# Kernel tuning notes

Hardware: AMD Instinct MI355X
Metric: run time of the kernel (lower is better)

The kernel has to match this reference:

```python
import jax, jax.numpy as jnp
import numpy as np


def _ortho_matrix(key, d, m):
    # block-orthogonal random matrix with chi-distributed row-norm rescaling
    n_blocks = m // d + (1 if m % d else 0)
    keys = jax.random.split(key, n_blocks + 1)
    blocks = []
    for i in range(m // d):
        q, _ = jnp.linalg.qr(jax.random.normal(keys[i], (d, d), dtype=jnp.float32))
        blocks.append(q)
    rem = m % d
    if rem > 0:
        q, _ = jnp.linalg.qr(jax.random.normal(keys[m // d], (d, d), dtype=jnp.float32))
        blocks.append(q[:, :rem])
    proj = jnp.concatenate(blocks, axis=1)  # [d, m]
    scales = jnp.linalg.norm(jax.random.normal(keys[-1], (m, d), dtype=jnp.float32), axis=1)
    return proj * scales[None, :]


def _feature_map(x, P, eps=1e-6):
    # FAVOR+ positive softmax feature map: [exp(xP - |x|^2/2), exp(-xP - |x|^2/2)]
    proj = x @ P  # [B,N,m]
    xn = 0.5 * jnp.sum(x * x, axis=-1, keepdims=True)
    pos = proj - xn
    neg = -proj - xn
    mx = jnp.maximum(jnp.max(pos, axis=-1, keepdims=True), jnp.max(neg, axis=-1, keepdims=True))
    feats = jnp.concatenate([jnp.exp(pos - mx), jnp.exp(neg - mx)], axis=-1)
    return feats * (2.0 * P.shape[1]) ** -0.5 + eps  # [B,N,2m]


def setup_inputs() -> dict:
    key = jax.random.key(0)
    ks = jax.random.split(key, 16)
    B, C, N = 4, 256, 8192
    da, nb = C // 4, 64
    d_geo, r_geo = 16, 16
    x = jax.random.normal(ks[0], (B, C, N), dtype=jnp.float32)
    pos = jax.random.uniform(ks[1], (B, N, 3), dtype=jnp.float32)
    Wq = jax.random.normal(ks[2], (da, C), dtype=jnp.float32) * (C ** -0.5)
    Wk = jax.random.normal(ks[3], (da, C), dtype=jnp.float32) * (C ** -0.5)
    Wv = jax.random.normal(ks[4], (C, C), dtype=jnp.float32) * (C ** -0.5)
    proj_sm = _ortho_matrix(ks[5], da, nb)  # [da, nb]
    Wg1 = jax.random.normal(ks[6], (d_geo, 3), dtype=jnp.float32) * (3 ** -0.5)
    bg1 = jnp.zeros((d_geo,), dtype=jnp.float32)
    Wg2 = jax.random.normal(ks[7], (d_geo, d_geo), dtype=jnp.float32) * (d_geo ** -0.5)
    bg2 = jnp.zeros((d_geo,), dtype=jnp.float32)
    log_tau = jnp.zeros((), dtype=jnp.float32)
    omega_geo = _ortho_matrix(ks[8], d_geo, r_geo)  # [d_geo, r_geo]
    Wp = jax.random.normal(ks[9], (C, C), dtype=jnp.float32) * (C ** -0.5)
    bn_gamma = jnp.ones((C,), dtype=jnp.float32)
    bn_beta = jnp.zeros((C,), dtype=jnp.float32)
    return {"x": x, "pos": pos, "Wq": Wq, "Wk": Wk, "Wv": Wv, "proj_sm": proj_sm,
            "Wg1": Wg1, "bg1": bg1, "Wg2": Wg2, "bg2": bg2, "log_tau": log_tau,
            "omega_geo": omega_geo, "Wp": Wp, "bn_gamma": bn_gamma, "bn_beta": bn_beta}


def reference(x, pos, Wq, Wk, Wv, proj_sm, Wg1, bg1, Wg2, bg2, log_tau, omega_geo, Wp, bn_gamma, bn_beta):
    eps = 1e-6
    da = Wq.shape[0]
    scale = da ** -0.25
    # 1x1 convs == channel matmuls; transpose to [B,N,*]
    q = jnp.einsum('bcn,oc->bno', x, Wq) * scale
    k = jnp.einsum('bcn,oc->bno', x, Wk) * scale
    v = jnp.einsum('bcn,oc->bno', x, Wv)
    q_p = _feature_map(q, proj_sm, eps)  # [B,N,r_sm]
    k_p = _feature_map(k, proj_sm, eps)
    # GeoRFF: learnable Gaussian RFF on MLP-transformed coordinates
    g = jax.nn.relu(pos @ Wg1.T + bg1) @ Wg2.T + bg2  # [B,N,d_geo]
    tau = jax.nn.softplus(log_tau) + 1e-6
    z = jnp.sqrt(2.0 * tau) * g
    z_proj = z @ omega_geo  # [B,N,r_geo]
    z_norm = 0.5 * jnp.sum(z * z, axis=-1, keepdims=True)
    phi = jnp.exp(z_proj - z_norm) * (omega_geo.shape[1] ** -0.5)  # [B,N,r_geo]
    # outer-product feature combination
    B, N, r_sm = q_p.shape
    r_geo = phi.shape[-1]
    Phi_q = (q_p[..., :, None] * phi[..., None, :]).reshape(B, N, r_sm * r_geo)
    Phi_k = (k_p[..., :, None] * phi[..., None, :]).reshape(B, N, r_sm * r_geo)
    # O(N) linear-attention chain
    kv = jnp.einsum('bnr,bnc->brc', Phi_k, v)         # [B,r,C]
    k_sum = jnp.sum(Phi_k, axis=1)                     # [B,r]
    denom = jnp.einsum('bnr,br->bn', Phi_q, k_sum)[..., None] + eps
    fsa = jnp.einsum('bnr,brc->bnc', Phi_q, kv) / denom  # [B,N,C]
    # offset attention: proj(x - fsa) + x, proj = Conv1x1 -> BN(train stats) -> ReLU
    y = x - jnp.transpose(fsa, (0, 2, 1))  # [B,C,N]
    h = jnp.einsum('bcn,oc->bon', y, Wp)
    mean = jnp.mean(h, axis=(0, 2), keepdims=True)
    var = jnp.var(h, axis=(0, 2), keepdims=True)
    hn = (h - mean) * jax.lax.rsqrt(var + 1e-5) * bn_gamma[None, :, None] + bn_beta[None, :, None]
    return jax.nn.relu(hn) + x
```

## Files before the change

kernel.cpp:

```cpp
#include <hip/hip_runtime.h>
#include <hip/hip_bf16.h>
#include <math.h>

#define BB 4
#define CC 256
#define NN 8192
#define RSM 128
#define RGEO 16

typedef __attribute__((ext_vector_type(8))) short short8v;
typedef __attribute__((ext_vector_type(4))) float f32x4;
typedef __attribute__((ext_vector_type(4))) unsigned int u32x4;

#define MFMA16 __builtin_amdgcn_mfma_f32_16x16x32_bf16

#define P_QP   0ull
#define P_KPT  8388608ull
#define P_PHIR 16777216ull
#define P_PHIT 17825792ull
#define P_XT   18874368ull
#define P_VT   35651584ull
#define P_YNT  35651584ull
#define P_KVT  52428800ull
#define P_KVF  56623104ull
#define P_KSUM 65011712ull
#define P_DEN  65044480ull
#define P_WQK  65175552ull
#define P_WV   65241088ull
#define P_WP   65372160ull
#define P_PSMT 65503232ull
#define P_BN   65511424ull
#define P_H    0ull

__device__ __forceinline__ unsigned short f2bu(float f){
    __hip_bfloat16 h = __float2bfloat16(f);
    return __builtin_bit_cast(unsigned short, h);
}
__device__ __forceinline__ float bu2f(unsigned short u){
    return __builtin_bit_cast(float, ((unsigned int)u) << 16);
}
__device__ __forceinline__ unsigned int pack2(float a, float b){
    return (unsigned int)f2bu(a) | (((unsigned int)f2bu(b)) << 16);
}
__device__ __forceinline__ int swz128(int row, int cb){ return (row*128 + cb) ^ ((row & 7) << 4); }
__device__ __forceinline__ int swz256(int row, int cb){ return (row*256 + cb) ^ ((row & 7) << 4); }

__device__ __forceinline__ unsigned int bmul2(unsigned int uk, unsigned int up, float& ksacc){
    float lo = __builtin_bit_cast(float, uk << 16) * __builtin_bit_cast(float, up << 16);
    float hi = __builtin_bit_cast(float, uk & 0xffff0000u) * __builtin_bit_cast(float, up & 0xffff0000u);
    ksacc += lo + hi;
    return pack2(lo, hi);
}

__device__ __forceinline__ void stage64(const unsigned short* __restrict__ g, size_t stride,
                                        char* lds, int t){
    #pragma unroll
    for (int i = 0; i < 2; ++i){
        int id = t + 256*i; int row = id >> 3, q = id & 7;
        short8v v = *(const short8v*)(g + (size_t)row*stride + q*8);
        *(short8v*)(lds + swz128(row, q*16)) = v;
    }
}
__device__ __forceinline__ short8v fld(const char* lds, int row, int cb){
    return *(const short8v*)(lds + swz128(row, cb));
}
__device__ __forceinline__ void mfma8(const char* As, const char* Bs, f32x4 acc[2][2],
                                      int wm, int wn, int lr, int lq){
    #pragma unroll
    for (int kk = 0; kk < 2; ++kk){
        short8v a0 = fld(As, wm*32 + lr,      kk*64 + lq*16);
        short8v a1 = fld(As, wm*32 + 16 + lr, kk*64 + lq*16);
        short8v b0 = fld(Bs, wn*32 + lr,      kk*64 + lq*16);
        short8v b1 = fld(Bs, wn*32 + 16 + lr, kk*64 + lq*16);
        acc[0][0] = MFMA16(a0, b0, acc[0][0], 0, 0, 0);
        acc[0][1] = MFMA16(a0, b1, acc[0][1], 0, 0, 0);
        acc[1][0] = MFMA16(a1, b0, acc[1][0], 0, 0, 0);
        acc[1][1] = MFMA16(a1, b1, acc[1][1], 0, 0, 0);
    }
}
__device__ __forceinline__ void mfma16s(const char* As, const char* Bs, f32x4 acc[4][4],
                                        int wm, int wn, int lr, int lq){
    #pragma unroll
    for (int kk = 0; kk < 2; ++kk){
        short8v af[4], bf[4];
        #pragma unroll
        for (int f = 0; f < 4; ++f) af[f] = fld(As, wm*64 + f*16 + lr, kk*64 + lq*16);
        #pragma unroll
        for (int f = 0; f < 4; ++f) bf[f] = fld(Bs, wn*64 + f*16 + lr, kk*64 + lq*16);
        #pragma unroll
        for (int fa = 0; fa < 4; ++fa)
            #pragma unroll
            for (int fb = 0; fb < 4; ++fb)
                acc[fa][fb] = MFMA16(af[fa], bf[fb], acc[fa][fb], 0, 0, 0);
    }
}
__device__ __forceinline__ void mfma4x2(const char* As, const char* Bs, f32x4 acc[4][2],
                                        int wm, int wn, int lr, int lq){
    #pragma unroll
    for (int kk = 0; kk < 2; ++kk){
        short8v af[4], bf[2];
        #pragma unroll
        for (int f = 0; f < 4; ++f) af[f] = fld(As, wm*64 + f*16 + lr, kk*64 + lq*16);
        #pragma unroll
        for (int f = 0; f < 2; ++f) bf[f] = fld(Bs, wn*32 + f*16 + lr, kk*64 + lq*16);
        #pragma unroll
        for (int fa = 0; fa < 4; ++fa)
            #pragma unroll
            for (int fb = 0; fb < 2; ++fb)
                acc[fa][fb] = MFMA16(af[fa], bf[fb], acc[fa][fb], 0, 0, 0);
    }
}

__global__ __launch_bounds__(256) void k_prep(const float* __restrict__ Wq, const float* __restrict__ Wk,
    const float* __restrict__ Wv, const float* __restrict__ Wp, const float* __restrict__ Psm,
    unsigned short* __restrict__ Wqk_bf, unsigned short* __restrict__ Wv_bf,
    unsigned short* __restrict__ Wp_bf, unsigned short* __restrict__ Psm_t)
{
    const int tid = blockIdx.x*256 + threadIdx.x;
    const int nth = 64*256;
    for (int i = tid; i < 32768; i += nth){
        int o = i >> 8, c = i & 255;
        Wqk_bf[i] = f2bu(o < 64 ? Wq[o*256 + c] : Wk[(o-64)*256 + c]);
    }
    for (int i = tid; i < 65536; i += nth) Wv_bf[i] = f2bu(Wv[i]);
    for (int i = tid; i < 65536; i += nth) Wp_bf[i] = f2bu(Wp[i]);
    for (int i = tid; i < 4096; i += nth){
        int m = i >> 6, o = i & 63;
        Psm_t[i] = f2bu(Psm[o*64 + m] * 0.35355339059327373f);
    }
}

__global__ __launch_bounds__(256) void k_xt(const float* __restrict__ x, unsigned short* __restrict__ xT)
{
    __shared__ float xs[64][65];
    const int t = threadIdx.x;
    const int b  = blockIdx.x >> 9;
    const int ct = (blockIdx.x >> 7) & 3;
    const int nt = blockIdx.x & 127;
    const int c0 = ct*64, n0 = nt*64;
    #pragma unroll
    for (int i = 0; i < 4; ++i){
        int id = t + 256*i; int row = id >> 4, fq = id & 15;
        f32x4 v = *(const f32x4*)(x + ((size_t)(b*CC + c0 + row))*NN + n0 + fq*4);
        xs[row][fq*4+0] = v[0]; xs[row][fq*4+1] = v[1];
        xs[row][fq*4+2] = v[2]; xs[row][fq*4+3] = v[3];
    }
    __syncthreads();
    #pragma unroll
    for (int i = 0; i < 2; ++i){
        int id = t + 256*i; int n = id >> 3, q = id & 7;
        u32x4 o;
        #pragma unroll
        for (int j2 = 0; j2 < 4; ++j2)
            o[j2] = pack2(xs[q*8 + j2*2][n], xs[q*8 + j2*2+1][n]);
        *(u32x4*)(void*)(xT + ((size_t)(b*NN + n0 + n))*CC + c0 + q*8) = o;
    }
}

__global__ __launch_bounds__(256) void k_wgemm(const unsigned short* __restrict__ A,
    const unsigned short* __restrict__ Bsrc, unsigned short* __restrict__ out, int orows)
{
    __shared__ __align__(16) char As[8192];
    __shared__ __align__(16) char Bs[8192];
    const int t = threadIdx.x;
    const int l = t & 63, w = t >> 6, wm = w >> 1, wn = w & 1, lr = l & 15, lq = l >> 4;
    const int b  = blockIdx.x >> 9;
    const int ct = (blockIdx.x >> 7) & 3;
    const int nt = blockIdx.x & 127;
    const int c0 = ct*64, n0 = nt*64;

    f32x4 acc[2][2] = {};
    for (int ks = 0; ks < 4; ++ks){
        stage64(A + (size_t)c0*256 + ks*64, 256, As, t);
        stage64(Bsrc + ((size_t)(b*NN + n0))*256 + ks*64, 256, Bs, t);
        __syncthreads();
        mfma8(As, Bs, acc, wm, wn, lr, lq);
        __syncthreads();
    }
    #pragma unroll
    for (int mi = 0; mi < 2; ++mi)
        #pragma unroll
        for (int ni = 0; ni < 2; ++ni)
            #pragma unroll
            for (int r = 0; r < 4; ++r){
                int c = c0 + wm*32 + mi*16 + lq*4 + r;
                int n = n0 + wn*32 + ni*16 + lr;
                out[((size_t)(b*orows + c))*NN + n] = f2bu(acc[mi][ni][r]);
            }
}

__global__ __launch_bounds__(256) void k_qk(const unsigned short* __restrict__ Wqk,
    const unsigned short* __restrict__ xT, const unsigned short* __restrict__ Psm_t,
    unsigned short* __restrict__ qp, unsigned short* __restrict__ kp_t)
{
    __shared__ __align__(16) char As[16384];
    __shared__ __align__(16) char Bs[8192];
    __shared__ __align__(16) char Ts[16384];
    __shared__ __align__(16) char Ps[8192];
    const int t = threadIdx.x;
    const int l = t & 63, w = t >> 6, wm = w >> 1, wn = w & 1, lr = l & 15, lq = l >> 4;
    const int b  = blockIdx.x >> 7;
    const int nt = blockIdx.x & 127;
    const int n0 = nt*64;

    stage64(Psm_t, 64, Ps, t);

    f32x4 acc[4][2] = {};
    for (int ks = 0; ks < 4; ++ks){
        #pragma unroll
        for (int i = 0; i < 4; ++i){
            int id = t + 256*i; int row = id >> 3, q = id & 7;
            short8v v = *(const short8v*)(Wqk + (size_t)row*256 + ks*64 + q*8);
            *(short8v*)(As + swz128(row, q*16)) = v;
        }
        stage64(xT + ((size_t)(b*NN + n0))*256 + ks*64, 256, Bs, t);
        __syncthreads();
        #pragma unroll
        for (int kk = 0; kk < 2; ++kk){
            short8v b0 = fld(Bs, wn*32 + lr,      kk*64 + lq*16);
            short8v b1 = fld(Bs, wn*32 + 16 + lr, kk*64 + lq*16);
            #pragma unroll
            for (int mi = 0; mi < 4; ++mi){
                short8v a = fld(As, wm*64 + mi*16 + lr, kk*64 + lq*16);
                acc[mi][0] = MFMA16(a, b0, acc[mi][0], 0, 0, 0);
                acc[mi][1] = MFMA16(a, b1, acc[mi][1], 0, 0, 0);
            }
        }
        __syncthreads();
    }
    #pragma unroll
    for (int mi = 0; mi < 4; ++mi)
        #pragma unroll
        for (int ni = 0; ni < 2; ++ni){
            int op = (wm*64 + mi*16 + lq*4)*2;
            int nrow = wn*32 + ni*16 + lr;
            *(unsigned int*)(Ts + swz256(nrow, op))     = pack2(acc[mi][ni][0], acc[mi][ni][1]);
            *(unsigned int*)(Ts + swz256(nrow, op + 4)) = pack2(acc[mi][ni][2], acc[mi][ni][3]);
        }
    __syncthreads();

    const float inv128 = 0.08838834764831845f;
    for (int p = 0; p < 2; ++p){
        f32x4 ac[4] = {};
        #pragma unroll
        for (int kk = 0; kk < 2; ++kk){
            short8v bf = *(const short8v*)(Ts + swz256(w*16 + lr, p*128 + kk*64 + lq*16));
            #pragma unroll
            for (int mi = 0; mi < 4; ++mi){
                short8v a = *(const short8v*)(Ps + swz128(mi*16 + lr, kk*64 + lq*16));
                ac[mi] = MFMA16(a, bf, ac[mi], 0, 0, 0);
            }
        }
        float mx = 0.f;
        #pragma unroll
        for (int mi = 0; mi < 4; ++mi)
            #pragma unroll
            for (int r = 0; r < 4; ++r) mx = fmaxf(mx, fabsf(ac[mi][r]));
        mx = fmaxf(mx, __shfl_xor(mx, 16));
        mx = fmaxf(mx, __shfl_xor(mx, 32));
        const int n = n0 + w*16 + lr;
        if (p == 0){
            unsigned short* qr = qp + ((size_t)(b*NN + n))*RSM;
            #pragma unroll
            for (int mi = 0; mi < 4; ++mi){
                float e0 = __expf( ac[mi][0]-mx)*inv128 + 1e-6f;
                float e1 = __expf( ac[mi][1]-mx)*inv128 + 1e-6f;
                float e2 = __expf( ac[mi][2]-mx)*inv128 + 1e-6f;
                float e3 = __expf( ac[mi][3]-mx)*inv128 + 1e-6f;
                float g0 = __expf(-ac[mi][0]-mx)*inv128 + 1e-6f;
                float g1 = __expf(-ac[mi][1]-mx)*inv128 + 1e-6f;
                float g2 = __expf(-ac[mi][2]-mx)*inv128 + 1e-6f;
                float g3 = __expf(-ac[mi][3]-mx)*inv128 + 1e-6f;
                int i0 = mi*16 + lq*4;
                uint2 pu; pu.x = pack2(e0, e1); pu.y = pack2(e2, e3);
                uint2 nu; nu.x = pack2(g0, g1); nu.y = pack2(g2, g3);
                *(uint2*)(void*)(qr + i0)      = pu;
                *(uint2*)(void*)(qr + 64 + i0) = nu;
            }
        } else {
            unsigned short* kb = kp_t + (size_t)(b*RSM)*NN + n;
            #pragma unroll
            for (int mi = 0; mi < 4; ++mi){
                int i0 = mi*16 + lq*4;
                #pragma unroll
                for (int r = 0; r < 4; ++r){
                    kb[(size_t)(i0 + r)*NN]      = f2bu(__expf( ac[mi][r]-mx)*inv128 + 1e-6f);
                    kb[(size_t)(i0 + r + 64)*NN] = f2bu(__expf(-ac[mi][r]-mx)*inv128 + 1e-6f);
                }
            }
        }
    }
}

__global__ __launch_bounds__(256) void k_phi(const float* __restrict__ pos,
    const float* __restrict__ Wg1, const float* __restrict__ bg1,
    const float* __restrict__ Wg2, const float* __restrict__ bg2,
    const float* __restrict__ log_tau, const float* __restrict__ omega,
    unsigned short* __restrict__ phi_row, unsigned short* __restrict__ phi_t)
{
    const int t = threadIdx.x;
    const int b = blockIdx.x >> 5;
    const int n = ((blockIdx.x & 31) << 8) + t;
    const float* pp = pos + ((size_t)(b*NN + n))*3;
    const float p0 = pp[0], p1 = pp[1], p2 = pp[2];
    float hb[16];
    #pragma unroll
    for (int i = 0; i < 16; ++i)
        hb[i] = fmaxf(0.f, fmaf(Wg1[i*3+0], p0, fmaf(Wg1[i*3+1], p1, fmaf(Wg1[i*3+2], p2, bg1[i]))));
    const float tau = log1pf(__expf(log_tau[0])) + 1e-6f;
    const float sc  = sqrtf(2.f*tau);
    float z[16]; float zn = 0.f;
    #pragma unroll
    for (int i = 0; i < 16; ++i){
        float g = bg2[i];
        #pragma unroll
        for (int j = 0; j < 16; ++j) g = fmaf(Wg2[i*16+j], hb[j], g);
        z[i] = sc*g; zn = fmaf(z[i], z[i], zn);
    }
    zn *= 0.5f;
    float val[16];
    #pragma unroll
    for (int m = 0; m < 16; ++m){
        float s = 0.f;
        #pragma unroll
        for (int i = 0; i < 16; ++i) s = fmaf(z[i], omega[i*16+m], s);
        val[m] = __expf(s - zn)*0.25f;
    }
    unsigned short* pr = phi_row + ((size_t)(b*NN + n))*16;
    u32x4 o0, o1;
    #pragma unroll
    for (int j2 = 0; j2 < 4; ++j2){
        o0[j2] = pack2(val[j2*2], val[j2*2+1]);
        o1[j2] = pack2(val[8+j2*2], val[8+j2*2+1]);
    }
    *(u32x4*)(void*)pr = o0;
    *(u32x4*)(void*)(pr + 8) = o1;
    #pragma unroll
    for (int m = 0; m < 16; ++m)
        phi_t[((size_t)(b*RGEO + m))*NN + n] = f2bu(val[m]);
}

__global__ __launch_bounds__(256) void k_kv(const unsigned short* __restrict__ kp_t,
    const unsigned short* __restrict__ phi_t, const unsigned short* __restrict__ v_t,
    float* __restrict__ kv_f32, float* __restrict__ ksum)
{
    __shared__ __align__(16) char As[16384];
    __shared__ __align__(16) char Bs[16384];
    const int t = threadIdx.x;
    const int l = t & 63, w = t >> 6, wm = w >> 1, wn = w & 1, lr = l & 15, lq = l >> 4;
    const int bid = blockIdx.x;
    const int rt  = bid & 15;
    const int ct  = (bid >> 4) & 1;
    const int ksl = (bid >> 5) & 15;
    const int b   = bid >> 9;
    const int c0 = ct*128, r0 = rt*128;

    const int arow = t >> 3, aq = t & 7;
    const int brow = t >> 1, half = t & 1;
    const int rg = r0 + brow;
    const unsigned short* kpr = kp_t + ((size_t)(b*RSM  + (rg >> 4)))*NN;
    const unsigned short* phr = phi_t + ((size_t)(b*RGEO + (rg & 15)))*NN;
    const unsigned short* vb  = v_t + ((size_t)(b*CC + c0))*NN;
    float ksacc = 0.f;

    short8v vA[4];
    unsigned int ob[16];
    int nk = ksl*512;

    #pragma unroll
    for (int i = 0; i < 4; ++i)
        vA[i] = *(const short8v*)(vb + (size_t)(arow + 32*i)*NN + nk + aq*8);
    #pragma unroll
    for (int g2 = 0; g2 < 4; ++g2){
        u32x4 uk = __builtin_bit_cast(u32x4, *(const short8v*)(kpr + nk + half*32 + g2*8));
        u32x4 up = __builtin_bit_cast(u32x4, *(const short8v*)(phr + nk + half*32 + g2*8));
        #pragma unroll
        for (int j = 0; j < 4; ++j) ob[g2*4 + j] = bmul2(uk[j], up[j], ksacc);
    }

    f32x4 acc[4][4] = {};
    for (int ks = 0; ks < 8; ++ks){
        __syncthreads();
        #pragma unroll
        for (int i = 0; i < 4; ++i)
            *(short8v*)(As + swz128(arow + 32*i, aq*16)) = vA[i];
        #pragma unroll
        for (int g2 = 0; g2 < 4; ++g2){
            u32x4 o; o[0]=ob[g2*4]; o[1]=ob[g2*4+1]; o[2]=ob[g2*4+2]; o[3]=ob[g2*4+3];
            *(u32x4*)(Bs + swz128(brow, half*64 + g2*16)) = o;
        }
        if (ks < 7){
            nk += 64;
            #pragma unroll
            for (int i = 0; i < 4; ++i)
                vA[i] = *(const short8v*)(vb + (size_t)(arow + 32*i)*NN + nk + aq*8);
            #pragma unroll
            for (int g2 = 0; g2 < 4; ++g2){
                u32x4 uk = __builtin_bit_cast(u32x4, *(const short8v*)(kpr + nk + half*32 + g2*8));
                u32x4 up = __builtin_bit_cast(u32x4, *(const short8v*)(phr + nk + half*32 + g2*8));
                #pragma unroll
                for (int j = 0; j < 4; ++j) ob[g2*4 + j] = bmul2(uk[j], up[j], ksacc);
            }
        }
        __syncthreads();
        mfma16s(As, Bs, acc, wm, wn, lr, lq);
    }
    #pragma unroll
    for (int fa = 0; fa < 4; ++fa)
        #pragma unroll
        for (int fb = 0; fb < 4; ++fb)
            #pragma unroll
            for (int e = 0; e < 4; ++e){
                int c = c0 + wm*64 + fa*16 + lq*4 + e;
                int r = r0 + wn*64 + fb*16 + lr;
                atomicAdd(&kv_f32[((size_t)(b*CC + c))*2048 + r], acc[fa][fb][e]);
            }
    if (ct == 0){
        float o = __shfl_xor(ksacc, 1);
        if (half == 0) atomicAdd(&ksum[b*2048 + rg], ksacc + o);
    }
}

__global__ __launch_bounds__(256) void k_kvred(const float* __restrict__ kv_f32,
    unsigned short* __restrict__ kv_t)
{
    const size_t i = ((size_t)blockIdx.x*256 + threadIdx.x)*4;
    f32x4 v = *(const f32x4*)(kv_f32 + i);
    uint2 o; o.x = pack2(v[0], v[1]); o.y = pack2(v[2], v[3]);
    *(uint2*)(void*)(kv_t + i) = o;
}

__global__ __launch_bounds__(256) void k_denom(const unsigned short* __restrict__ qp,
    const unsigned short* __restrict__ phi_row, const float* __restrict__ ksum,
    float* __restrict__ den)
{
    __shared__ float ks[2048];
    const int t = threadIdx.x;
    const int b = blockIdx.x >> 5;
    const int n = ((blockIdx.x & 31) << 8) + t;
    const float* ksrc = ksum + b*2048;
    #pragma unroll
    for (int i = 0; i < 8; ++i){ int idx = t + 256*i; ks[idx] = ksrc[idx]; }
    __syncthreads();
    float phf[16];
    {
        const unsigned short* pr = phi_row + ((size_t)(b*NN + n))*16;
        short8v a = *(const short8v*)pr;
        short8v c = *(const short8v*)(pr + 8);
        #pragma unroll
        for (int j = 0; j < 8; ++j){ phf[j] = bu2f((unsigned short)a[j]); phf[8+j] = bu2f((unsigned short)c[j]); }
    }
    const unsigned short* qr = qp + ((size_t)(b*NN + n))*RSM;
    float acc = 0.f;
    for (int i = 0; i < 128; i += 8){
        short8v qv = *(const short8v*)(qr + i);
        #pragma unroll
        for (int ii = 0; ii < 8; ++ii){
            const float* kk = &ks[(i + ii)*16];
            float s = 0.f;
            #pragma unroll
            for (int j = 0; j < 16; ++j) s = fmaf(phf[j], kk[j], s);
            acc = fmaf(bu2f((unsigned short)qv[ii]), s, acc);
        }
    }
    den[b*NN + n] = acc + 1e-6f;
}

__global__ __launch_bounds__(256) void k_fsa(const unsigned short* __restrict__ kv_t,
    const unsigned short* __restrict__ qp, const unsigned short* __restrict__ phi_row,
    const float* __restrict__ den, const unsigned short* __restrict__ xT,
    unsigned short* __restrict__ y_nt)
{
    __shared__ __align__(16) char Sm[24576];
    char* As = Sm;
    char* Bs = Sm + 16384;
    const int t = threadIdx.x;
    const int l = t & 63, w = t >> 6, wm = w >> 1, wn = w & 1, lr = l & 15, lq = l >> 4;
    const int nt = blockIdx.x & 127;
    const int ct = (blockIdx.x >> 7) & 1;
    const int b  = blockIdx.x >> 8;
    const int c0 = ct*128, n0 = nt*64;

    const int arow = t >> 3, aq = t & 7;
    const int brow = t >> 2, quarter = t & 3;
    float phf[16];
    {
        const unsigned short* pr = phi_row + ((size_t)(b*NN + n0 + brow))*16;
        short8v a = *(const short8v*)pr;
        short8v c = *(const short8v*)(pr + 8);
        #pragma unroll
        for (int j = 0; j < 8; ++j){ phf[j] = bu2f((unsigned short)a[j]); phf[8+j] = bu2f((unsigned short)c[j]); }
    }
    const unsigned short* qrow = qp + ((size_t)(b*NN + n0 + brow))*RSM;
    const unsigned short* kvb  = kv_t + ((size_t)(b*CC + c0))*2048;

    short8v vA[4];
    float qv;
    int rk = 0;
    #pragma unroll
    for (int i = 0; i < 4; ++i)
        vA[i] = *(const short8v*)(kvb + (size_t)(arow + 32*i)*2048 + rk + aq*8);
    qv = bu2f(qrow[(rk >> 4) + quarter]);

    f32x4 acc[4][2] = {};
    for (int ks = 0; ks < 32; ++ks){
        u32x4 o0, o1;
        #pragma unroll
        for (int j2 = 0; j2 < 4; ++j2){
            o0[j2] = pack2(qv*phf[j2*2],     qv*phf[j2*2+1]);
            o1[j2] = pack2(qv*phf[8+j2*2],   qv*phf[8+j2*2+1]);
        }
        __syncthreads();
        #pragma unroll
        for (int i = 0; i < 4; ++i)
            *(short8v*)(As + swz128(arow + 32*i, aq*16)) = vA[i];
        *(u32x4*)(Bs + swz128(brow, quarter*32))      = o0;
        *(u32x4*)(Bs + swz128(brow, quarter*32 + 16)) = o1;
        if (ks < 31){
            rk += 64;
            #pragma unroll
            for (int i = 0; i < 4; ++i)
                vA[i] = *(const short8v*)(kvb + (size_t)(arow + 32*i)*2048 + rk + aq*8);
            qv = bu2f(qrow[(rk >> 4) + quarter]);
        }
        __syncthreads();
        mfma4x2(As, Bs, acc, wm, wn, lr, lq);
    }
    __syncthreads();
    float rd[2];
    #pragma unroll
    for (int fb = 0; fb < 2; ++fb)
        rd[fb] = 1.0f / den[(size_t)b*NN + n0 + wn*32 + fb*16 + lr];
    #pragma unroll
    for (int fa = 0; fa < 4; ++fa)
        #pragma unroll
        for (int fb = 0; fb < 2; ++fb){
            int nrow = wn*32 + fb*16 + lr;
            int cb   = (wm*64 + fa*16 + lq*4)*2;
            *(unsigned int*)(Sm + swz256(nrow, cb))     = pack2(acc[fa][fb][0]*rd[fb], acc[fa][fb][1]*rd[fb]);
            *(unsigned int*)(Sm + swz256(nrow, cb + 4)) = pack2(acc[fa][fb][2]*rd[fb], acc[fa][fb][3]*rd[fb]);
        }
    __syncthreads();
    #pragma unroll
    for (int i = 0; i < 4; ++i){
        int id = t + 256*i; int row = id >> 4, q = id & 15;
        short8v fs = *(const short8v*)(Sm + swz256(row, q*16));
        short8v xv = *(const short8v*)(xT + ((size_t)(b*NN + n0 + row))*CC + c0 + q*8);
        u32x4 o;
        #pragma unroll
        for (int j2 = 0; j2 < 4; ++j2){
            float y0 = bu2f((unsigned short)xv[j2*2])   - bu2f((unsigned short)fs[j2*2]);
            float y1 = bu2f((unsigned short)xv[j2*2+1]) - bu2f((unsigned short)fs[j2*2+1]);
            o[j2] = pack2(y0, y1);
        }
        *(u32x4*)(void*)(y_nt + ((size_t)(b*NN + n0 + row))*CC + c0 + q*8) = o;
    }
}

__global__ __launch_bounds__(256) void k_bnstat(const unsigned short* __restrict__ h,
    const float* __restrict__ gamma, const float* __restrict__ beta, float* __restrict__ bn)
{
    __shared__ float s1[256], s2[256];
    const int t = threadIdx.x, c = blockIdx.x;
    float a1 = 0.f, a2 = 0.f;
    for (int b = 0; b < 4; ++b){
        const unsigned short* hr = h + ((size_t)(b*CC + c))*NN;
        #pragma unroll
        for (int i = 0; i < 4; ++i){
            short8v v = *(const short8v*)(hr + (t + i*256)*8);
            #pragma unroll
            for (int j = 0; j < 8; ++j){ float f = bu2f((unsigned short)v[j]); a1 += f; a2 = fmaf(f, f, a2); }
        }
    }
    s1[t] = a1; s2[t] = a2; __syncthreads();
    for (int st = 128; st > 0; st >>= 1){
        if (t < st){ s1[t] += s1[t + st]; s2[t] += s2[t + st]; }
        __syncthreads();
    }
    if (t == 0){
        float inv = 1.f/32768.f;
        float mean = s1[0]*inv, var = s2[0]*inv - mean*mean;
        float sc = gamma[c]*rsqrtf(var + 1e-5f);
        bn[512 + c] = sc; bn[768 + c] = fmaf(-mean, sc, beta[c]);
    }
}

__global__ __launch_bounds__(256) void k_apply(const unsigned short* __restrict__ h,
    const float* __restrict__ x, const float* __restrict__ bn, float* __restrict__ out)
{
    const size_t tot8 = (size_t)BB*CC*NN/8;
    for (size_t i = (size_t)blockIdx.x*256 + threadIdx.x; i < tot8; i += 2048*256){
        int c = (int)((i >> 10) & 255);
        float s = bn[512 + c], bb = bn[768 + c];
        short8v hv = *(const short8v*)(h + i*8);
        f32x4 x0 = *(const f32x4*)(x + i*8);
        f32x4 x1 = *(const f32x4*)(x + i*8 + 4);
        f32x4 o0, o1;
        #pragma unroll
        for (int j = 0; j < 4; ++j){
            o0[j] = fmaxf(fmaf(bu2f((unsigned short)hv[j]),     s, bb), 0.f) + x0[j];
            o1[j] = fmaxf(fmaf(bu2f((unsigned short)hv[4 + j]), s, bb), 0.f) + x1[j];
        }
        *(f32x4*)(out + i*8)     = o0;
        *(f32x4*)(out + i*8 + 4) = o1;
    }
}

extern "C" void kernel_launch(void* const* d_in, const int* in_sizes, int n_in,
                              void* d_out, int out_size, void* d_ws, size_t ws_size,
                              hipStream_t stream)
{
    (void)in_sizes; (void)n_in; (void)out_size; (void)ws_size;
    const float* x       = (const float*)d_in[0];
    const float* pos     = (const float*)d_in[1];
    const float* Wq      = (const float*)d_in[2];
    const float* Wk      = (const float*)d_in[3];
    const float* Wv      = (const float*)d_in[4];
    const float* Psm     = (const float*)d_in[5];
    const float* Wg1     = (const float*)d_in[6];
    const float* bg1     = (const float*)d_in[7];
    const float* Wg2     = (const float*)d_in[8];
    const float* bg2     = (const float*)d_in[9];
    const float* log_tau = (const float*)d_in[10];
    const float* omega   = (const float*)d_in[11];
    const float* Wp      = (const float*)d_in[12];
    const float* gamma   = (const float*)d_in[13];
    const float* beta    = (const float*)d_in[14];
    char* W = (char*)d_ws;
    float* out = (float*)d_out;

    unsigned short* qp    = (unsigned short*)(W + P_QP);
    unsigned short* kp_t  = (unsigned short*)(W + P_KPT);
    unsigned short* phir  = (unsigned short*)(W + P_PHIR);
    unsigned short* phit  = (unsigned short*)(W + P_PHIT);
    unsigned short* xT    = (unsigned short*)(W + P_XT);
    unsigned short* v_t   = (unsigned short*)(W + P_VT);
    unsigned short* y_nt  = (unsigned short*)(W + P_YNT);
    unsigned short* kv_t  = (unsigned short*)(W + P_KVT);
    float*          kvf   = (float*)(W + P_KVF);
    float*          ksum  = (float*)(W + P_KSUM);
    float*          den   = (float*)(W + P_DEN);
    unsigned short* Wqk_b = (unsigned short*)(W + P_WQK);
    unsigned short* Wv_b  = (unsigned short*)(W + P_WV);
    unsigned short* Wp_b  = (unsigned short*)(W + P_WP);
    unsigned short* Psm_t = (unsigned short*)(W + P_PSMT);
    float*          bn    = (float*)(W + P_BN);
    unsigned short* hbuf  = (unsigned short*)(W + P_H);

    hipMemsetAsync(W + P_KVF, 0, 8421376, stream);
    k_prep  <<<  64, 256, 0, stream>>>(Wq, Wk, Wv, Wp, Psm, Wqk_b, Wv_b, Wp_b, Psm_t);
    k_xt    <<<2048, 256, 0, stream>>>(x, xT);
    k_wgemm <<<2048, 256, 0, stream>>>(Wv_b, xT, v_t, 256);
    k_qk    <<< 512, 256, 0, stream>>>(Wqk_b, xT, Psm_t, qp, kp_t);
    k_phi   <<< 128, 256, 0, stream>>>(pos, Wg1, bg1, Wg2, bg2, log_tau, omega, phir, phit);
    k_kv    <<<2048, 256, 0, stream>>>(kp_t, phit, v_t, kvf, ksum);
    k_kvred <<<2048, 256, 0, stream>>>(kvf, kv_t);
    k_denom <<< 128, 256, 0, stream>>>(qp, phir, ksum, den);
    k_fsa   <<<1024, 256, 0, stream>>>(kv_t, qp, phir, den, xT, y_nt);
    k_wgemm <<<2048, 256, 0, stream>>>(Wp_b, y_nt, hbuf, 256);
    k_bnstat<<< 256, 256, 0, stream>>>(hbuf, gamma, beta, bn);
    k_apply <<<2048, 256, 0, stream>>>(hbuf, x, bn, out);
}
```

Before: 353.3 us.

## Fuse denominator into fsa kernel and halve kv split-K blocks

Removes the separate k_denom kernel. Each k_fsa block now loads ksum into shared memory, accumulates the denominator from the same q·phi products it already builds for the MFMA operand, and reduces it across lanes with shuffles. Separately, k_kv now covers 1024 tokens per block instead of 512 and launches half as many blocks, which halves the atomicAdd traffic into the fp32 kv buffer. The cost is extra per-iteration FMAs and 8KB more LDS in fsa, which may lower occupancy, plus a longer serial loop with fewer blocks in k_kv.

```diff
diff --git a/kernel.cpp b/kernel.cpp
--- a/kernel.cpp
+++ b/kernel.cpp
@@ -24,7 +24,6 @@
 #define P_KVT  52428800ull
 #define P_KVF  56623104ull
 #define P_KSUM 65011712ull
-#define P_DEN  65044480ull
 #define P_WQK  65175552ull
 #define P_WV   65241088ull
 #define P_WP   65372160ull
@@ -351,8 +350,8 @@
     const int bid = blockIdx.x;
     const int rt  = bid & 15;
     const int ct  = (bid >> 4) & 1;
-    const int ksl = (bid >> 5) & 15;
-    const int b   = bid >> 9;
+    const int ksl = (bid >> 5) & 7;
+    const int b   = bid >> 8;
     const int c0 = ct*128, r0 = rt*128;
 
     const int arow = t >> 3, aq = t & 7;
@@ -365,7 +364,7 @@
 
     short8v vA[4];
     unsigned int ob[16];
-    int nk = ksl*512;
+    int nk = ksl*1024;
 
     #pragma unroll
     for (int i = 0; i < 4; ++i)
@@ -379,7 +378,7 @@
     }
 
     f32x4 acc[4][4] = {};
-    for (int ks = 0; ks < 8; ++ks){
+    for (int ks = 0; ks < 16; ++ks){
         __syncthreads();
         #pragma unroll
         for (int i = 0; i < 4; ++i)
@@ -389,7 +388,7 @@
             u32x4 o; o[0]=ob[g2*4]; o[1]=ob[g2*4+1]; o[2]=ob[g2*4+2]; o[3]=ob[g2*4+3];
             *(u32x4*)(Bs + swz128(brow, half*64 + g2*16)) = o;
         }
-        if (ks < 7){
+        if (ks < 15){
             nk += 64;
             #pragma unroll
             for (int i = 0; i < 4; ++i)
@@ -430,48 +429,14 @@
     *(uint2*)(void*)(kv_t + i) = o;
 }
 
-__global__ __launch_bounds__(256) void k_denom(const unsigned short* __restrict__ qp,
-    const unsigned short* __restrict__ phi_row, const float* __restrict__ ksum,
-    float* __restrict__ den)
-{
-    __shared__ float ks[2048];
-    const int t = threadIdx.x;
-    const int b = blockIdx.x >> 5;
-    const int n = ((blockIdx.x & 31) << 8) + t;
-    const float* ksrc = ksum + b*2048;
-    #pragma unroll
-    for (int i = 0; i < 8; ++i){ int idx = t + 256*i; ks[idx] = ksrc[idx]; }
-    __syncthreads();
-    float phf[16];
-    {
-        const unsigned short* pr = phi_row + ((size_t)(b*NN + n))*16;
-        short8v a = *(const short8v*)pr;
-        short8v c = *(const short8v*)(pr + 8);
-        #pragma unroll
-        for (int j = 0; j < 8; ++j){ phf[j] = bu2f((unsigned short)a[j]); phf[8+j] = bu2f((unsigned short)c[j]); }
-    }
-    const unsigned short* qr = qp + ((size_t)(b*NN + n))*RSM;
-    float acc = 0.f;
-    for (int i = 0; i < 128; i += 8){
-        short8v qv = *(const short8v*)(qr + i);
-        #pragma unroll
-        for (int ii = 0; ii < 8; ++ii){
-            const float* kk = &ks[(i + ii)*16];
-            float s = 0.f;
-            #pragma unroll
-            for (int j = 0; j < 16; ++j) s = fmaf(phf[j], kk[j], s);
-            acc = fmaf(bu2f((unsigned short)qv[ii]), s, acc);
-        }
-    }
-    den[b*NN + n] = acc + 1e-6f;
-}
-
 __global__ __launch_bounds__(256) void k_fsa(const unsigned short* __restrict__ kv_t,
     const unsigned short* __restrict__ qp, const unsigned short* __restrict__ phi_row,
-    const float* __restrict__ den, const unsigned short* __restrict__ xT,
+    const float* __restrict__ ksum, const unsigned short* __restrict__ xT,
     unsigned short* __restrict__ y_nt)
 {
     __shared__ __align__(16) char Sm[24576];
+    __shared__ float ksld[2048];
+    __shared__ float denb[64];
     char* As = Sm;
     char* Bs = Sm + 16384;
     const int t = threadIdx.x;
@@ -494,6 +459,9 @@
     const unsigned short* qrow = qp + ((size_t)(b*NN + n0 + brow))*RSM;
     const unsigned short* kvb  = kv_t + ((size_t)(b*CC + c0))*2048;
 
+    #pragma unroll
+    for (int i = 0; i < 8; ++i){ int idx = t + 256*i; ksld[idx] = ksum[b*2048 + idx]; }
+
     short8v vA[4];
     float qv;
     int rk = 0;
@@ -501,14 +469,33 @@
     for (int i = 0; i < 4; ++i)
         vA[i] = *(const short8v*)(kvb + (size_t)(arow + 32*i)*2048 + rk + aq*8);
     qv = bu2f(qrow[(rk >> 4) + quarter]);
-
+    __syncthreads();
+
+    float den_acc = 0.f;
     f32x4 acc[4][2] = {};
     for (int ks = 0; ks < 32; ++ks){
+        float pv[16];
+        #pragma unroll
+        for (int j = 0; j < 16; ++j) pv[j] = qv*phf[j];
+        {
+            const float* kr = &ksld[rk + quarter*16];
+            f32x4 k0 = *(const f32x4*)(kr);
+            f32x4 k1 = *(const f32x4*)(kr + 4);
+            f32x4 k2 = *(const f32x4*)(kr + 8);
+            f32x4 k3 = *(const f32x4*)(kr + 12);
+            #pragma unroll
+            for (int j = 0; j < 4; ++j){
+                den_acc = fmaf(pv[j],      k0[j], den_acc);
+                den_acc = fmaf(pv[4 + j],  k1[j], den_acc);
+                den_acc = fmaf(pv[8 + j],  k2[j], den_acc);
+                den_acc = fmaf(pv[12 + j], k3[j], den_acc);
+            }
+        }
         u32x4 o0, o1;
         #pragma unroll
         for (int j2 = 0; j2 < 4; ++j2){
-            o0[j2] = pack2(qv*phf[j2*2],     qv*phf[j2*2+1]);
-            o1[j2] = pack2(qv*phf[8+j2*2],   qv*phf[8+j2*2+1]);
+            o0[j2] = pack2(pv[j2*2],     pv[j2*2+1]);
+            o1[j2] = pack2(pv[8+j2*2],   pv[8+j2*2+1]);
         }
         __syncthreads();
         #pragma unroll
@@ -526,11 +513,14 @@
         __syncthreads();
         mfma4x2(As, Bs, acc, wm, wn, lr, lq);
     }
+    den_acc += __shfl_xor(den_acc, 1);
+    den_acc += __shfl_xor(den_acc, 2);
+    if (quarter == 0) denb[brow] = 1.0f / (den_acc + 1e-6f);
     __syncthreads();
     float rd[2];
     #pragma unroll
     for (int fb = 0; fb < 2; ++fb)
-        rd[fb] = 1.0f / den[(size_t)b*NN + n0 + wn*32 + fb*16 + lr];
+        rd[fb] = denb[wn*32 + fb*16 + lr];
     #pragma unroll
     for (int fa = 0; fa < 4; ++fa)
         #pragma unroll
@@ -639,7 +629,6 @@
     unsigned short* kv_t  = (unsigned short*)(W + P_KVT);
     float*          kvf   = (float*)(W + P_KVF);
     float*          ksum  = (float*)(W + P_KSUM);
-    float*          den   = (float*)(W + P_DEN);
     unsigned short* Wqk_b = (unsigned short*)(W + P_WQK);
     unsigned short* Wv_b  = (unsigned short*)(W + P_WV);
     unsigned short* Wp_b  = (unsigned short*)(W + P_WP);
@@ -653,10 +642,9 @@
     k_wgemm <<<2048, 256, 0, stream>>>(Wv_b, xT, v_t, 256);
     k_qk    <<< 512, 256, 0, stream>>>(Wqk_b, xT, Psm_t, qp, kp_t);
     k_phi   <<< 128, 256, 0, stream>>>(pos, Wg1, bg1, Wg2, bg2, log_tau, omega, phir, phit);
-    k_kv    <<<2048, 256, 0, stream>>>(kp_t, phit, v_t, kvf, ksum);
+    k_kv    <<<1024, 256, 0, stream>>>(kp_t, phit, v_t, kvf, ksum);
     k_kvred <<<2048, 256, 0, stream>>>(kvf, kv_t);
-    k_denom <<< 128, 256, 0, stream>>>(qp, phir, ksum, den);
-    k_fsa   <<<1024, 256, 0, stream>>>(kv_t, qp, phir, den, xT, y_nt);
+    k_fsa   <<<1024, 256, 0, stream>>>(kv_t, qp, phir, ksum, xT, y_nt);
     k_wgemm <<<2048, 256, 0, stream>>>(Wp_b, y_nt, hbuf, 256);
     k_bnstat<<< 256, 256, 0, stream>>>(hbuf, gamma, beta, bn);
     k_apply <<<2048, 256, 0, stream>>>(hbuf, x, bn, out);
```

Measured after the change: 318.1 us. -10.0%, faster.
